# Kernel optimization log

Hardware: AMD Instinct MI355X
Metric: run time of the kernel (lower is better)

## Reference

```python
import jax, jax.numpy as jnp
import numpy as np

DIM, DEPTH, DH, CH, SH = 512, 2, 64, 2, 8
B, T, N = 8, 1024, 2048
CI, SI, FF = CH * DH, SH * DH, 4 * DIM


def layer_norm(x, w, b, eps=1e-5):
    m = jnp.mean(x, -1, keepdims=True)
    v = jnp.var(x, -1, keepdims=True)
    return (x - m) * jax.lax.rsqrt(v + eps) * w + b


def rotate_half(x):
    # interleaved pairs: (x0,x1) -> (-x1,x0)
    x1, x2 = x[..., 0::2], x[..., 1::2]
    return jnp.stack((-x2, x1), axis=-1).reshape(x.shape)


def apply_rot(freqs, x):
    return x * jnp.cos(freqs) + rotate_half(x) * jnp.sin(freqs)


def split_heads(x, h):
    b, t, _ = x.shape
    return x.reshape(b, t, h, -1).transpose(0, 2, 1, 3)


def merge_heads(x):
    b, h, t, d = x.shape
    return x.transpose(0, 2, 1, 3).reshape(b, t, h * d)


def rotary_attn(q, k, v, q_pos, k_pos, heads, mask=None):
    # q:(B,Tq,H*Dh), k/v:(B,Tk,H*Dh), pos:(B,T,Dh); rotate_value=False -> v untouched
    qh, kh, vh = split_heads(q, heads), split_heads(k, heads), split_heads(v, heads)
    qh = apply_rot(q_pos[:, None], qh)
    kh = apply_rot(k_pos[:, None], kh)
    scores = jnp.einsum('bhqd,bhkd->bhqk', qh, kh) * (DH ** -0.5)
    if mask is not None:
        scores = jnp.where(mask, scores, jnp.finfo(scores.dtype).min)
    attn = jax.nn.softmax(scores, axis=-1)
    return merge_heads(jnp.einsum('bhqk,bhkd->bhqd', attn, vh))


def _forward(bin_queries, bin_time_emb, encoder_latents, latent_time_emb,
             ca_lnq_w, ca_lnq_b, ca_lnc_w, ca_lnc_b, ca_wq, ca_wkv, ca_wo, ca_bo,
             sa_ln_w, sa_ln_b, sa_wqkv, sa_wo, sa_bo,
             ffn_ln_w, ffn_ln_b, ffn_w1, ffn_b1, ffn_w2, ffn_b2):
    Tq = bin_queries.shape[1]
    mask = jnp.tril(jnp.ones((Tq, Tq), dtype=bool))[None, None]  # (1,1,T,T) causal
    x = bin_queries
    for l in range(DEPTH):
        # 1) rotary cross-attention to history latents
        xn = layer_norm(x, ca_lnq_w[l], ca_lnq_b[l])
        cn = layer_norm(encoder_latents, ca_lnc_w[l], ca_lnc_b[l])
        q = xn @ ca_wq[l]
        k, v = jnp.split(cn @ ca_wkv[l], 2, axis=-1)
        x = x + rotary_attn(q, k, v, bin_time_emb, latent_time_emb, CH) @ ca_wo[l] + ca_bo[l]
        # 2) causal rotary self-attention over bin queries
        xn = layer_norm(x, sa_ln_w[l], sa_ln_b[l])
        q, k, v = jnp.split(xn @ sa_wqkv[l], 3, axis=-1)
        x = x + rotary_attn(q, k, v, bin_time_emb, bin_time_emb, SH, mask) @ sa_wo[l] + sa_bo[l]
        # 3) pre-LN FFN with GEGLU (mult=4), dropout off in eval
        h = layer_norm(x, ffn_ln_w[l], ffn_ln_b[l])
        a, g = jnp.split(h @ ffn_w1[l] + ffn_b1[l], 2, axis=-1)
        x = x + (a * jax.nn.gelu(g, approximate=False)) @ ffn_w2[l] + ffn_b2[l]
    return x


def setup_inputs() -> dict:
    key = jax.random.key(0)
    ks = jax.random.split(key, 12)
    n = lambda i, shape, s: jax.random.normal(ks[i], shape, dtype=jnp.float32) * s
    return {
        'bin_queries': n(0, (B, T, DIM), 1.0),
        'bin_time_emb': n(1, (B, T, DH), 1.0),
        'encoder_latents': n(2, (B, N, DIM), 1.0),
        'latent_time_emb': n(3, (B, N, DH), 1.0),
        'ca_lnq_w': jnp.ones((DEPTH, DIM)), 'ca_lnq_b': jnp.zeros((DEPTH, DIM)),
        'ca_lnc_w': jnp.ones((DEPTH, DIM)), 'ca_lnc_b': jnp.zeros((DEPTH, DIM)),
        'ca_wq': n(4, (DEPTH, DIM, CI), 0.02), 'ca_wkv': n(5, (DEPTH, DIM, 2 * CI), 0.02),
        'ca_wo': n(6, (DEPTH, CI, DIM), 0.02), 'ca_bo': jnp.zeros((DEPTH, DIM)),
        'sa_ln_w': jnp.ones((DEPTH, DIM)), 'sa_ln_b': jnp.zeros((DEPTH, DIM)),
        'sa_wqkv': n(7, (DEPTH, DIM, 3 * SI), 0.02), 'sa_wo': n(8, (DEPTH, SI, DIM), 0.02),
        'sa_bo': jnp.zeros((DEPTH, DIM)),
        'ffn_ln_w': jnp.ones((DEPTH, DIM)), 'ffn_ln_b': jnp.zeros((DEPTH, DIM)),
        'ffn_w1': n(9, (DEPTH, DIM, 2 * FF), 0.02), 'ffn_b1': jnp.zeros((DEPTH, 2 * FF)),
        'ffn_w2': n(10, (DEPTH, FF, DIM), 0.02), 'ffn_b2': jnp.zeros((DEPTH, DIM)),
    }


def reference(bin_queries, bin_time_emb, encoder_latents, latent_time_emb,
              ca_lnq_w, ca_lnq_b, ca_lnc_w, ca_lnc_b, ca_wq, ca_wkv, ca_wo, ca_bo,
              sa_ln_w, sa_ln_b, sa_wqkv, sa_wo, sa_bo,
              ffn_ln_w, ffn_ln_b, ffn_w1, ffn_b1, ffn_w2, ffn_b2):
    return _forward(bin_queries, bin_time_emb, encoder_latents, latent_time_emb,
                    ca_lnq_w, ca_lnq_b, ca_lnc_w, ca_lnc_b, ca_wq, ca_wkv, ca_wo, ca_bo,
                    sa_ln_w, sa_ln_b, sa_wqkv, sa_wo, sa_bo,
                    ffn_ln_w, ffn_ln_b, ffn_w1, ffn_b1, ffn_w2, ffn_b2)
```

## Files before the change

kernel.cpp:

```cpp
#include <hip/hip_runtime.h>
#include <cstdint>
#include <cstddef>

static constexpr int DIMc = 512;
static constexpr int DHc  = 64;
static constexpr int CHc  = 2;
static constexpr int SHc  = 8;
static constexpr int Bc   = 8;
static constexpr int Tc   = 1024;
static constexpr int Nc   = 2048;
static constexpr int CIc  = CHc * DHc;
static constexpr int SIc  = SHc * DHc;
static constexpr int FFc  = 4 * DIMc;
static constexpr int RQ   = Bc * Tc;
static constexpr int RL   = Bc * Nc;

typedef short bf16x8 __attribute__((ext_vector_type(8)));
typedef float f32x4  __attribute__((ext_vector_type(4)));

__device__ __forceinline__ ushort f2bf(float f) {
  uint32_t u = __builtin_bit_cast(uint32_t, f);
  u += 0x7fffu + ((u >> 16) & 1u);
  return (ushort)(u >> 16);
}
__device__ __forceinline__ uint32_t packbf2(float a, float b) {
  return (uint32_t)f2bf(a) | ((uint32_t)f2bf(b) << 16);
}
__device__ __forceinline__ float bf2f(ushort h) {
  uint32_t u = ((uint32_t)h) << 16;
  return __builtin_bit_cast(float, u);
}

__device__ __forceinline__ void gload_lds16(const ushort* g, ushort* lds) {
  __builtin_amdgcn_global_load_lds(
      (const __attribute__((address_space(1))) void*)g,
      (__attribute__((address_space(3))) void*)lds, 16, 0, 0);
}

__device__ __forceinline__ float gelu_fast(float g) {
  float u = g * (0.7978845608f + 0.0356774081f * g * g);
  float e = __expf(2.f * u);
  float th = 1.f - 2.f * __builtin_amdgcn_rcpf(1.f + e);
  return 0.5f * g * (1.f + th);
}

__global__ __launch_bounds__(256) void ln_rows(const float* __restrict__ X,
    const float* __restrict__ w, const float* __restrict__ b,
    ushort* __restrict__ out, int rows) {
  int gw = (int)((blockIdx.x * 256 + threadIdx.x) >> 6);
  int lane = threadIdx.x & 63;
  if (gw >= rows) return;
  const float* xr = X + (size_t)gw * DIMc;
  float4 v0 = *(const float4*)(xr + lane * 8);
  float4 v1 = *(const float4*)(xr + lane * 8 + 4);
  float xv[8] = {v0.x, v0.y, v0.z, v0.w, v1.x, v1.y, v1.z, v1.w};
  float s = 0.f, ss = 0.f;
#pragma unroll
  for (int i = 0; i < 8; i++) { s += xv[i]; ss += xv[i] * xv[i]; }
#pragma unroll
  for (int off = 32; off; off >>= 1) { s += __shfl_xor(s, off); ss += __shfl_xor(ss, off); }
  float mean = s * (1.f / DIMc);
  float var = ss * (1.f / DIMc) - mean * mean;
  float r = rsqrtf(var + 1e-5f);
  int c = lane * 8;
  ushort o[8] __attribute__((aligned(16)));
#pragma unroll
  for (int i = 0; i < 8; i++) o[i] = f2bf((xv[i] - mean) * r * w[c + i] + b[c + i]);
  *(uint4*)(out + (size_t)gw * DIMc + c) = *(const uint4*)o;
}

__global__ __launch_bounds__(256) void wtrans_all(
    const float* __restrict__ wq, const float* __restrict__ wkv,
    const float* __restrict__ wo, const float* __restrict__ qkv,
    const float* __restrict__ swo, const float* __restrict__ w1,
    const float* __restrict__ w2, ushort* __restrict__ dst, int layer) {
  constexpr int Ks[7]   = {512, 512, 128, 512, 512, 512, 2048};
  constexpr int Ns[7]   = {128, 256, 512, 1536, 512, 4096, 512};
  constexpr int pre[8]  = {0, 64, 192, 256, 1024, 1280, 3328, 4352};
  constexpr int dOff[7] = {0, 65536, 196608, 262144, 1048576, 1310720, 3407872};
  int bid = blockIdx.x;
  int wid = 0;
#pragma unroll
  for (int i = 1; i < 7; i++) wid += (bid >= pre[i]);
  int tileIdx = bid - pre[wid];
  int K = Ks[wid], N = Ns[wid];
  const float* srcs[7] = {wq, wkv, wo, qkv, swo, w1, w2};
  const float* W = srcs[wid] + (size_t)layer * K * N;
  ushort* Wt = dst + dOff[wid];
  int ntx = N / 32;
  int n0 = (tileIdx % ntx) * 32, k0 = (tileIdx / ntx) * 32;
  __shared__ float tile[32][33];
  int tx = threadIdx.x & 31, ty = threadIdx.x >> 5;
#pragma unroll
  for (int i = 0; i < 32; i += 8)
    tile[ty + i][tx] = W[(size_t)(k0 + ty + i) * N + n0 + tx];
  __syncthreads();
  if (wid == 5) {
#pragma unroll
    for (int i = 0; i < 32; i += 8) {
      int nrow = n0 + ty + i;
      int p = nrow & 2047;
      int rowT = ((p >> 4) << 5) + ((nrow < 2048) ? 0 : 16) + (p & 15);
      Wt[(size_t)rowT * K + k0 + tx] = f2bf(tile[tx][ty + i]);
    }
  } else {
#pragma unroll
    for (int i = 0; i < 32; i += 8)
      Wt[(size_t)(n0 + ty + i) * K + k0 + tx] = f2bf(tile[tx][ty + i]);
  }
}

__global__ __launch_bounds__(256) void vtrans(const ushort* __restrict__ src,
    ushort* __restrict__ dst, int NK, int stride, int colOff) {
  __shared__ ushort tile[32][33];
  int b = blockIdx.z;
  int key0 = blockIdx.x * 32, hd0 = blockIdx.y * 32;
  int HD = gridDim.y * 32;
  int tx = threadIdx.x & 31, ty = threadIdx.x >> 5;
#pragma unroll
  for (int i = 0; i < 32; i += 8)
    tile[ty + i][tx] = src[(size_t)(b * NK + key0 + ty + i) * stride + colOff + hd0 + tx];
  __syncthreads();
#pragma unroll
  for (int i = 0; i < 32; i += 8)
    dst[((size_t)b * HD + hd0 + ty + i) * NK + key0 + tx] = tile[tx][ty + i];
}

template<int MODE>
__global__ __launch_bounds__(256) void gemm128(const ushort* __restrict__ A,
    const ushort* __restrict__ Bt, const float* __restrict__ bias,
    const float* __restrict__ resIn, float* __restrict__ resOut,
    ushort* __restrict__ outB, int M, int N, int K) {
  __shared__ __align__(16) ushort As[128 * 64];
  __shared__ __align__(16) ushort Bs[128 * 64];
  int t = threadIdx.x, wv = t >> 6, lane = t & 63;
  int bm = blockIdx.y, bn = blockIdx.x;
  int fr = lane & 15, g = lane >> 4;
  int wr = (wv >> 1) * 64, wc = (wv & 1) * 64;
  int srow = wv * 32 + (lane >> 3);
  int sslot = lane & 7;
  const ushort* Abase = A + (size_t)(bm * 128) * K;
  const ushort* Bbase = Bt + (size_t)(bn * 128) * K;

  f32x4 acc[4][4] = {};
  for (int k0 = 0; k0 < K; k0 += 64) {
#pragma unroll
    for (int j = 0; j < 4; j++) {
      int r = srow + j * 8;
      int kc = sslot ^ (r & 7);
      gload_lds16(Abase + (size_t)r * K + k0 + kc * 8, As + (wv * 256 + j * 64) * 8);
      gload_lds16(Bbase + (size_t)r * K + k0 + kc * 8, Bs + (wv * 256 + j * 64) * 8);
    }
    __syncthreads();
#pragma unroll
    for (int ks = 0; ks < 2; ks++) {
      bf16x8 af[4], bf[4];
#pragma unroll
      for (int mm = 0; mm < 4; mm++) {
        int row = wr + mm * 16 + fr;
        af[mm] = *(const bf16x8*)(As + row * 64 + (((ks * 4 + g) ^ (row & 7)) * 8));
      }
#pragma unroll
      for (int nn = 0; nn < 4; nn++) {
        int row = wc + nn * 16 + fr;
        bf[nn] = *(const bf16x8*)(Bs + row * 64 + (((ks * 4 + g) ^ (row & 7)) * 8));
      }
#pragma unroll
      for (int mm = 0; mm < 4; mm++)
#pragma unroll
        for (int nn = 0; nn < 4; nn++)
          acc[mm][nn] = __builtin_amdgcn_mfma_f32_16x16x32_bf16(af[mm], bf[nn], acc[mm][nn], 0, 0, 0);
    }
    __syncthreads();
  }

  if (MODE == 2) {
    int NH = N >> 1;
#pragma unroll
    for (int mm = 0; mm < 4; mm++)
#pragma unroll
      for (int np = 0; np < 2; np++) {
        int ocol = bn * 64 + (wc >> 1) + np * 16 + fr;
        float ba = bias[ocol];
        float bg = bias[NH + ocol];
#pragma unroll
        for (int i = 0; i < 4; i++) {
          int gr = bm * 128 + wr + mm * 16 + g * 4 + i;
          float a = acc[mm][np * 2][i] + ba;
          float gv = acc[mm][np * 2 + 1][i] + bg;
          outB[(size_t)gr * NH + ocol] = f2bf(a * gelu_fast(gv));
        }
      }
  } else {
#pragma unroll
    for (int mm = 0; mm < 4; mm++)
#pragma unroll
      for (int nn = 0; nn < 4; nn++)
#pragma unroll
        for (int i = 0; i < 4; i++) {
          int gr = bm * 128 + wr + mm * 16 + g * 4 + i;
          int gc = bn * 128 + wc + nn * 16 + fr;
          float val = acc[mm][nn][i] + (bias ? bias[gc] : 0.f);
          if (MODE == 0) outB[(size_t)gr * N + gc] = f2bf(val);
          else resOut[(size_t)gr * N + gc] = resIn[(size_t)gr * N + gc] + val;
        }
  }
}

template<int MODE>
__global__ __launch_bounds__(256) void gemm128x64(const ushort* __restrict__ A,
    const ushort* __restrict__ Bt, const float* __restrict__ bias,
    const float* __restrict__ resIn, float* __restrict__ resOut,
    ushort* __restrict__ outB, int M, int N, int K) {
  __shared__ __align__(16) ushort As[128 * 64];
  __shared__ __align__(16) ushort Bs[64 * 64];
  int t = threadIdx.x, wv = t >> 6, lane = t & 63;
  int bm = blockIdx.y, bn = blockIdx.x;
  int fr = lane & 15, g = lane >> 4;
  int wr = (wv >> 1) * 64, wc = (wv & 1) * 32;
  const ushort* Abase = A + (size_t)(bm * 128) * K;
  const ushort* Bbase = Bt + (size_t)(bn * 64) * K;

  f32x4 acc[4][2] = {};
  for (int k0 = 0; k0 < K; k0 += 64) {
#pragma unroll
    for (int j = 0; j < 4; j++) {
      int c = j * 256 + wv * 64 + lane;
      int r = c >> 3, s = c & 7;
      int kc = s ^ (r & 7);
      gload_lds16(Abase + (size_t)r * K + k0 + kc * 8, As + (j * 256 + wv * 64) * 8);
      if (j < 2)
        gload_lds16(Bbase + (size_t)r * K + k0 + kc * 8, Bs + (j * 256 + wv * 64) * 8);
    }
    __syncthreads();
#pragma unroll
    for (int ks = 0; ks < 2; ks++) {
      bf16x8 af[4], bf[2];
#pragma unroll
      for (int mm = 0; mm < 4; mm++) {
        int row = wr + mm * 16 + fr;
        af[mm] = *(const bf16x8*)(As + row * 64 + (((ks * 4 + g) ^ (row & 7)) * 8));
      }
#pragma unroll
      for (int nn = 0; nn < 2; nn++) {
        int row = wc + nn * 16 + fr;
        bf[nn] = *(const bf16x8*)(Bs + row * 64 + (((ks * 4 + g) ^ (row & 7)) * 8));
      }
#pragma unroll
      for (int mm = 0; mm < 4; mm++)
#pragma unroll
        for (int nn = 0; nn < 2; nn++)
          acc[mm][nn] = __builtin_amdgcn_mfma_f32_16x16x32_bf16(af[mm], bf[nn], acc[mm][nn], 0, 0, 0);
    }
    __syncthreads();
  }

#pragma unroll
  for (int mm = 0; mm < 4; mm++)
#pragma unroll
    for (int nn = 0; nn < 2; nn++)
#pragma unroll
      for (int i = 0; i < 4; i++) {
        int gr = bm * 128 + wr + mm * 16 + g * 4 + i;
        int gc = bn * 64 + wc + nn * 16 + fr;
        float val = acc[mm][nn][i] + (bias ? bias[gc] : 0.f);
        if (MODE == 0) outB[(size_t)gr * N + gc] = f2bf(val);
        else resOut[(size_t)gr * N + gc] = resIn[(size_t)gr * N + gc] + val;
      }
}

template<int MODE>
__global__ __launch_bounds__(256) void gemm64(const ushort* __restrict__ A,
    const ushort* __restrict__ Bt, const float* __restrict__ bias,
    float* __restrict__ resF, ushort* __restrict__ outB,
    int M, int N, int K) {
  __shared__ __align__(16) ushort As[64][40];
  __shared__ __align__(16) ushort Bs[64][40];
  int t = threadIdx.x;
  int bm = blockIdx.y, bn = blockIdx.x;
  int row = t >> 2, kc = (t & 3) << 3;
  const ushort* aG = A + (size_t)(bm * 64 + row) * K + kc;
  const ushort* bG = Bt + (size_t)(bn * 64 + row) * K + kc;
  int wv = t >> 6, lane = t & 63;
  int wr = (wv >> 1) * 32, wc = (wv & 1) * 32;
  int fr = lane & 15, fk = (lane >> 4) << 3;
  f32x4 acc[2][2] = {};
  for (int k0 = 0; k0 < K; k0 += 32) {
    *(uint4*)&As[row][kc] = *(const uint4*)(aG + k0);
    *(uint4*)&Bs[row][kc] = *(const uint4*)(bG + k0);
    __syncthreads();
    bf16x8 a0 = *(const bf16x8*)&As[wr + fr][fk];
    bf16x8 a1 = *(const bf16x8*)&As[wr + 16 + fr][fk];
    bf16x8 b0 = *(const bf16x8*)&Bs[wc + fr][fk];
    bf16x8 b1 = *(const bf16x8*)&Bs[wc + 16 + fr][fk];
    acc[0][0] = __builtin_amdgcn_mfma_f32_16x16x32_bf16(a0, b0, acc[0][0], 0, 0, 0);
    acc[0][1] = __builtin_amdgcn_mfma_f32_16x16x32_bf16(a0, b1, acc[0][1], 0, 0, 0);
    acc[1][0] = __builtin_amdgcn_mfma_f32_16x16x32_bf16(a1, b0, acc[1][0], 0, 0, 0);
    acc[1][1] = __builtin_amdgcn_mfma_f32_16x16x32_bf16(a1, b1, acc[1][1], 0, 0, 0);
    __syncthreads();
  }
  int cr0 = wr + ((lane >> 4) << 2);
  int cc0 = wc + fr;
#pragma unroll
  for (int mm = 0; mm < 2; mm++)
#pragma unroll
    for (int nn = 0; nn < 2; nn++)
#pragma unroll
      for (int i = 0; i < 4; i++) {
        int gr = bm * 64 + cr0 + mm * 16 + i;
        int gc = bn * 64 + cc0 + nn * 16;
        float val = acc[mm][nn][i] + (bias ? bias[gc] : 0.f);
        if (MODE == 0) outB[(size_t)gr * N + gc] = f2bf(val);
        else resF[(size_t)gr * N + gc] = resF[(size_t)gr * N + gc] + val;
      }
}

__global__ __launch_bounds__(256) void rope_apply(ushort* __restrict__ buf,
    const float* __restrict__ fr, int rows, int stride, int colOff, int H, float scale) {
  int idx = blockIdx.x * 256 + threadIdx.x;
  int total = rows * H * 32;
  if (idx >= total) return;
  int p = idx & 31;
  int h = (idx >> 5) % H;
  int r = idx / (32 * H);
  float f0 = fr[(size_t)r * DHc + 2 * p];
  float f1 = fr[(size_t)r * DHc + 2 * p + 1];
  ushort* bp = buf + (size_t)r * stride + colOff + h * DHc + 2 * p;
  float x0 = bf2f(bp[0]), x1 = bf2f(bp[1]);
  float o0 = (x0 * __cosf(f0) - x1 * __sinf(f0)) * scale;
  float o1 = (x1 * __cosf(f1) + x0 * __sinf(f1)) * scale;
  bp[0] = f2bf(o0); bp[1] = f2bf(o1);
}

template<int CAUSAL>
__global__ __launch_bounds__(256) void attn_mfma(
    const ushort* __restrict__ Q, const ushort* __restrict__ K,
    const ushort* __restrict__ Vt, ushort* __restrict__ O,
    int qStride, int kStride, int kOff, int oStride,
    int Tq, int NK, int H) {
  __shared__ __align__(16) ushort Ks[64 * 64];
  __shared__ __align__(16) ushort Vs[64 * 64];
  __shared__ __align__(16) ushort Ps[4][16 * 72];
  int b = blockIdx.z, h = blockIdx.y;
  int qt = CAUSAL ? ((int)gridDim.x - 1 - (int)blockIdx.x) : blockIdx.x;
  int t = threadIdx.x, wv = t >> 6, lane = t & 63;
  int g = lane >> 4, fr = lane & 15;
  int qw = qt * 64 + wv * 16;
  int HD = H * 64;

  const ushort* qrow = Q + (size_t)(b * Tq + qw + fr) * qStride + h * 64;
  bf16x8 qlo = *(const bf16x8*)(qrow + g * 8);
  bf16x8 qhi = *(const bf16x8*)(qrow + 32 + g * 8);

  f32x4 o_acc[4] = {};
  float m_run = -1e30f, l_run = 0.f;

  uint32_t* Pw = (uint32_t*)&Ps[wv][0];
  int ntiles = CAUSAL ? (qt + 1) : (NK / 64);
  for (int kt = 0; kt < ntiles; kt++) {
    int k0 = kt * 64;
    __syncthreads();
#pragma unroll
    for (int i = 0; i < 2; i++) {
      int id = t + i * 256;
      int r = id >> 3, c = id & 7;
      uint4 kval = *(const uint4*)(K + (size_t)(b * NK + k0 + r) * kStride + kOff + h * 64 + c * 8);
      *(uint4*)(Ks + r * 64 + ((c ^ (r & 7)) * 8)) = kval;
      uint4 vval = *(const uint4*)(Vt + ((size_t)b * HD + h * 64 + r) * NK + k0 + c * 8);
      *(uint4*)(Vs + r * 64 + ((c ^ (r & 7)) * 8)) = vval;
    }
    __syncthreads();

    f32x4 s[4];
#pragma unroll
    for (int nn = 0; nn < 4; nn++) {
      int row = nn * 16 + fr;
      bf16x8 kf0 = *(const bf16x8*)(Ks + row * 64 + ((g ^ (fr & 7)) * 8));
      bf16x8 kf1 = *(const bf16x8*)(Ks + row * 64 + (((4 + g) ^ (fr & 7)) * 8));
      f32x4 z = {};
      z = __builtin_amdgcn_mfma_f32_16x16x32_bf16(kf0, qlo, z, 0, 0, 0);
      z = __builtin_amdgcn_mfma_f32_16x16x32_bf16(kf1, qhi, z, 0, 0, 0);
      s[nn] = z;
    }
    if (CAUSAL && (k0 + 63 > qw)) {
#pragma unroll
      for (int nn = 0; nn < 4; nn++)
#pragma unroll
        for (int i = 0; i < 4; i++)
          if (k0 + nn * 16 + g * 4 + i > qw + fr) s[nn][i] = -1e30f;
    }
    float tm = s[0][0];
#pragma unroll
    for (int nn = 0; nn < 4; nn++)
#pragma unroll
      for (int i = 0; i < 4; i++) tm = fmaxf(tm, s[nn][i]);
    tm = fmaxf(tm, __shfl_xor(tm, 16));
    tm = fmaxf(tm, __shfl_xor(tm, 32));
    float mnew = fmaxf(m_run, tm);
    float corr = __expf(m_run - mnew);
    float ps = 0.f;
#pragma unroll
    for (int nn = 0; nn < 4; nn++)
#pragma unroll
      for (int i = 0; i < 4; i++) {
        float p = __expf(s[nn][i] - mnew);
        s[nn][i] = p;
        ps += p;
      }
    ps += __shfl_xor(ps, 16);
    ps += __shfl_xor(ps, 32);
    l_run = l_run * corr + ps;
    m_run = mnew;
#pragma unroll
    for (int dd = 0; dd < 4; dd++) o_acc[dd] *= corr;
#pragma unroll
    for (int nn = 0; nn < 4; nn++)
#pragma unroll
      for (int p = 0; p < 2; p++)
        Pw[fr * 36 + 8 * nn + 2 * g + p] = packbf2(s[nn][2 * p], s[nn][2 * p + 1]);
    bf16x8 pa0 = *(const bf16x8*)(&Ps[wv][fr * 72 + g * 8]);
    bf16x8 pa1 = *(const bf16x8*)(&Ps[wv][fr * 72 + 32 + g * 8]);
#pragma unroll
    for (int dd = 0; dd < 4; dd++) {
      int row = dd * 16 + fr;
      bf16x8 vf0 = *(const bf16x8*)(Vs + row * 64 + ((g ^ (fr & 7)) * 8));
      bf16x8 vf1 = *(const bf16x8*)(Vs + row * 64 + (((4 + g) ^ (fr & 7)) * 8));
      o_acc[dd] = __builtin_amdgcn_mfma_f32_16x16x32_bf16(vf0, pa0, o_acc[dd], 0, 0, 0);
      o_acc[dd] = __builtin_amdgcn_mfma_f32_16x16x32_bf16(vf1, pa1, o_acc[dd], 0, 0, 0);
    }
  }
  float rl = 1.f / l_run;
  ushort* obase = O + (size_t)(b * Tq + qw + fr) * oStride + h * 64;
#pragma unroll
  for (int dd = 0; dd < 4; dd++) {
    uint2 w;
    w.x = packbf2(o_acc[dd][0] * rl, o_acc[dd][1] * rl);
    w.y = packbf2(o_acc[dd][2] * rl, o_acc[dd][3] * rl);
    *(uint2*)(obase + dd * 16 + g * 4) = w;
  }
}

extern "C" void kernel_launch(void* const* d_in, const int* in_sizes, int n_in,
                              void* d_out, int out_size, void* d_ws, size_t ws_size,
                              hipStream_t stream) {
  const float* bin_queries = (const float*)d_in[0];
  const float* bin_time    = (const float*)d_in[1];
  const float* latents     = (const float*)d_in[2];
  const float* lat_time    = (const float*)d_in[3];
  const float* ca_lnq_w = (const float*)d_in[4];
  const float* ca_lnq_b = (const float*)d_in[5];
  const float* ca_lnc_w = (const float*)d_in[6];
  const float* ca_lnc_b = (const float*)d_in[7];
  const float* ca_wq  = (const float*)d_in[8];
  const float* ca_wkv = (const float*)d_in[9];
  const float* ca_wo  = (const float*)d_in[10];
  const float* ca_bo  = (const float*)d_in[11];
  const float* sa_ln_w = (const float*)d_in[12];
  const float* sa_ln_b = (const float*)d_in[13];
  const float* sa_wqkv = (const float*)d_in[14];
  const float* sa_wo   = (const float*)d_in[15];
  const float* sa_bo   = (const float*)d_in[16];
  const float* ffn_ln_w = (const float*)d_in[17];
  const float* ffn_ln_b = (const float*)d_in[18];
  const float* ffn_w1 = (const float*)d_in[19];
  const float* ffn_b1 = (const float*)d_in[20];
  const float* ffn_w2 = (const float*)d_in[21];
  const float* ffn_b2 = (const float*)d_in[22];

  constexpr size_t X_BYTES = (size_t)RQ * DIMc * 4;
  char* ws = (char*)d_ws;
  float* x = (float*)ws;
  char* A0 = ws + X_BYTES;
  ushort* cn     = (ushort*)(A0);
  ushort* ca_xn  = (ushort*)(A0 + 16777216);
  ushort* qbuf   = (ushort*)(A0 + 25165824);
  ushort* kv     = (ushort*)(A0 + 27262976);
  ushort* ca_att = (ushort*)(A0 + 35651584);
  ushort* vt_c   = (ushort*)(A0 + 37748736);
  ushort* sa_xn  = (ushort*)(A0);
  ushort* qkv    = (ushort*)(A0 + 8388608);
  ushort* sa_att = (ushort*)(A0 + 33554432);
  ushort* vt_s   = (ushort*)(A0 + 41943040);
  ushort* hb     = (ushort*)(A0);
  ushort* ag     = (ushort*)(A0 + 8388608);
  char* W0 = A0 + 109051904;
  ushort* wbase = (ushort*)W0;
  ushort* wqT  = wbase;
  ushort* wkvT = wbase + 65536;
  ushort* woT  = wbase + 196608;
  ushort* qkvT = wbase + 262144;
  ushort* swoT = wbase + 1048576;
  ushort* w1T  = wbase + 1310720;
  ushort* w2T  = wbase + 3407872;

  hipMemcpyAsync(x, bin_queries, X_BYTES, hipMemcpyDeviceToDevice, stream);

  for (int l = 0; l < 2; l++) {
    wtrans_all<<<4352, 256, 0, stream>>>(ca_wq, ca_wkv, ca_wo, sa_wqkv, sa_wo,
                                         ffn_w1, ffn_w2, wbase, l);

    ln_rows<<<RQ / 4, 256, 0, stream>>>(x, ca_lnq_w + l * DIMc, ca_lnq_b + l * DIMc, ca_xn, RQ);
    ln_rows<<<RL / 4, 256, 0, stream>>>(latents, ca_lnc_w + l * DIMc, ca_lnc_b + l * DIMc, cn, RL);
    gemm64<0><<<dim3(CIc / 64, RQ / 64), 256, 0, stream>>>(ca_xn, wqT, nullptr, nullptr, qbuf, RQ, CIc, DIMc);
    gemm128x64<0><<<dim3(2 * CIc / 64, RL / 128), 256, 0, stream>>>(cn, wkvT, nullptr,
        nullptr, nullptr, kv, RL, 2 * CIc, DIMc);
    rope_apply<<<(RQ * CHc * 32) / 256, 256, 0, stream>>>(qbuf, bin_time, RQ, CIc, 0, CHc, 0.125f);
    rope_apply<<<(RL * CHc * 32) / 256, 256, 0, stream>>>(kv, lat_time, RL, 2 * CIc, 0, CHc, 1.f);
    vtrans<<<dim3(Nc / 32, CHc * 64 / 32, Bc), 256, 0, stream>>>(kv, vt_c, Nc, 2 * CIc, CIc);
    attn_mfma<0><<<dim3(Tc / 64, CHc, Bc), 256, 0, stream>>>(qbuf, kv, vt_c, ca_att,
        CIc, 2 * CIc, 0, CIc, Tc, Nc, CHc);
    gemm128x64<1><<<dim3(DIMc / 64, RQ / 128), 256, 0, stream>>>(ca_att, woT, ca_bo + l * DIMc,
        x, x, nullptr, RQ, DIMc, CIc);

    ln_rows<<<RQ / 4, 256, 0, stream>>>(x, sa_ln_w + l * DIMc, sa_ln_b + l * DIMc, sa_xn, RQ);
    gemm128<0><<<dim3(3 * SIc / 128, RQ / 128), 256, 0, stream>>>(sa_xn, qkvT, nullptr,
        nullptr, nullptr, qkv, RQ, 3 * SIc, DIMc);
    rope_apply<<<(RQ * SHc * 32) / 256, 256, 0, stream>>>(qkv, bin_time, RQ, 3 * SIc, 0, SHc, 0.125f);
    rope_apply<<<(RQ * SHc * 32) / 256, 256, 0, stream>>>(qkv, bin_time, RQ, 3 * SIc, SIc, SHc, 1.f);
    vtrans<<<dim3(Tc / 32, SHc * 64 / 32, Bc), 256, 0, stream>>>(qkv, vt_s, Tc, 3 * SIc, 2 * SIc);
    attn_mfma<1><<<dim3(Tc / 64, SHc, Bc), 256, 0, stream>>>(qkv, qkv, vt_s, sa_att,
        3 * SIc, 3 * SIc, SIc, SIc, Tc, Tc, SHc);
    gemm128x64<1><<<dim3(DIMc / 64, RQ / 128), 256, 0, stream>>>(sa_att, swoT, sa_bo + l * DIMc,
        x, x, nullptr, RQ, DIMc, SIc);

    ln_rows<<<RQ / 4, 256, 0, stream>>>(x, ffn_ln_w + l * DIMc, ffn_ln_b + l * DIMc, hb, RQ);
    gemm128<2><<<dim3(2 * FFc / 128, RQ / 128), 256, 0, stream>>>(hb, w1T,
        ffn_b1 + (size_t)l * 2 * FFc, nullptr, nullptr, ag, RQ, 2 * FFc, DIMc);
    float* resOut = (l == 1) ? (float*)d_out : x;
    gemm128x64<1><<<dim3(DIMc / 64, RQ / 128), 256, 0, stream>>>(ag, w2T, ffn_b2 + l * DIMc,
        x, resOut, nullptr, RQ, DIMc, FFc);
  }
}
```

Measured before the change: 685.7 us.

## Fuse rotary embedding and V transpose into projection GEMM epilogues

```diff
diff --git a/kernel.cpp b/kernel.cpp
--- a/kernel.cpp
+++ b/kernel.cpp
@@ -44,6 +44,19 @@
   return 0.5f * g * (1.f + th);
 }
 
+__device__ __forceinline__ float rope_rot(int odd, float v, float p, float2 cs) {
+  return odd ? (v * cs.x + p * cs.y) : (v * cs.x - p * cs.y);
+}
+
+__global__ __launch_bounds__(256) void trig_prep(const float* __restrict__ src,
+    float2* __restrict__ dst, int n) {
+  int i = blockIdx.x * 256 + threadIdx.x;
+  if (i >= n) return;
+  float s, c;
+  __sincosf(src[i], &s, &c);
+  dst[i] = make_float2(c, s);
+}
+
 __global__ __launch_bounds__(256) void ln_rows(const float* __restrict__ X,
     const float* __restrict__ w, const float* __restrict__ b,
     ushort* __restrict__ out, int rows) {
@@ -110,27 +123,12 @@
   }
 }
 
-__global__ __launch_bounds__(256) void vtrans(const ushort* __restrict__ src,
-    ushort* __restrict__ dst, int NK, int stride, int colOff) {
-  __shared__ ushort tile[32][33];
-  int b = blockIdx.z;
-  int key0 = blockIdx.x * 32, hd0 = blockIdx.y * 32;
-  int HD = gridDim.y * 32;
-  int tx = threadIdx.x & 31, ty = threadIdx.x >> 5;
-#pragma unroll
-  for (int i = 0; i < 32; i += 8)
-    tile[ty + i][tx] = src[(size_t)(b * NK + key0 + ty + i) * stride + colOff + hd0 + tx];
-  __syncthreads();
-#pragma unroll
-  for (int i = 0; i < 32; i += 8)
-    dst[((size_t)b * HD + hd0 + ty + i) * NK + key0 + tx] = tile[tx][ty + i];
-}
-
 template<int MODE>
 __global__ __launch_bounds__(256) void gemm128(const ushort* __restrict__ A,
     const ushort* __restrict__ Bt, const float* __restrict__ bias,
     const float* __restrict__ resIn, float* __restrict__ resOut,
-    ushort* __restrict__ outB, int M, int N, int K) {
+    ushort* __restrict__ outB, int M, int N, int K,
+    const float2* __restrict__ cs, ushort* __restrict__ vt) {
   __shared__ __align__(16) ushort As[128 * 64];
   __shared__ __align__(16) ushort Bs[128 * 64];
   int t = threadIdx.x, wv = t >> 6, lane = t & 63;
@@ -191,6 +189,39 @@
           outB[(size_t)gr * NH + ocol] = f2bf(a * gelu_fast(gv));
         }
       }
+  } else if (MODE == 3) {
+    if (bn * 128 < 1024) {
+#pragma unroll
+      for (int mm = 0; mm < 4; mm++)
+#pragma unroll
+        for (int nn = 0; nn < 4; nn++) {
+          int gc = bn * 128 + wc + nn * 16 + fr;
+          int d = gc & 63;
+          float sc = (gc < 512) ? 0.125f : 1.f;
+#pragma unroll
+          for (int i = 0; i < 4; i++) {
+            int gr = bm * 128 + wr + mm * 16 + g * 4 + i;
+            float val = acc[mm][nn][i];
+            float prt = __shfl_xor(val, 1);
+            float2 csv = cs[(size_t)gr * 64 + d];
+            outB[(size_t)gr * N + gc] = f2bf(rope_rot(fr & 1, val, prt, csv) * sc);
+          }
+        }
+    } else {
+#pragma unroll
+      for (int mm = 0; mm < 4; mm++)
+#pragma unroll
+        for (int nn = 0; nn < 4; nn++) {
+          int gc = bn * 128 + wc + nn * 16 + fr;
+          int ch = gc - 1024;
+          int gr0 = bm * 128 + wr + mm * 16 + g * 4;
+          int bb = gr0 >> 10, t0 = gr0 & 1023;
+          uint2 w;
+          w.x = packbf2(acc[mm][nn][0], acc[mm][nn][1]);
+          w.y = packbf2(acc[mm][nn][2], acc[mm][nn][3]);
+          *(uint2*)(vt + ((size_t)bb * 512 + ch) * 1024 + t0) = w;
+        }
+    }
   } else {
 #pragma unroll
     for (int mm = 0; mm < 4; mm++)
@@ -211,7 +242,8 @@
 __global__ __launch_bounds__(256) void gemm128x64(const ushort* __restrict__ A,
     const ushort* __restrict__ Bt, const float* __restrict__ bias,
     const float* __restrict__ resIn, float* __restrict__ resOut,
-    ushort* __restrict__ outB, int M, int N, int K) {
+    ushort* __restrict__ outB, int M, int N, int K,
+    const float2* __restrict__ cs, ushort* __restrict__ vt) {
   __shared__ __align__(16) ushort As[128 * 64];
   __shared__ __align__(16) ushort Bs[64 * 64];
   int t = threadIdx.x, wv = t >> 6, lane = t & 63;
@@ -255,25 +287,57 @@
     __syncthreads();
   }
 
-#pragma unroll
-  for (int mm = 0; mm < 4; mm++)
-#pragma unroll
-    for (int nn = 0; nn < 2; nn++)
-#pragma unroll
-      for (int i = 0; i < 4; i++) {
-        int gr = bm * 128 + wr + mm * 16 + g * 4 + i;
-        int gc = bn * 64 + wc + nn * 16 + fr;
-        float val = acc[mm][nn][i] + (bias ? bias[gc] : 0.f);
-        if (MODE == 0) outB[(size_t)gr * N + gc] = f2bf(val);
-        else resOut[(size_t)gr * N + gc] = resIn[(size_t)gr * N + gc] + val;
-      }
-}
-
-template<int MODE>
-__global__ __launch_bounds__(256) void gemm64(const ushort* __restrict__ A,
-    const ushort* __restrict__ Bt, const float* __restrict__ bias,
-    float* __restrict__ resF, ushort* __restrict__ outB,
-    int M, int N, int K) {
+  if (MODE == 3) {
+    if (bn * 64 < 128) {
+#pragma unroll
+      for (int mm = 0; mm < 4; mm++)
+#pragma unroll
+        for (int nn = 0; nn < 2; nn++) {
+          int gc = bn * 64 + wc + nn * 16 + fr;
+          int d = gc & 63;
+#pragma unroll
+          for (int i = 0; i < 4; i++) {
+            int gr = bm * 128 + wr + mm * 16 + g * 4 + i;
+            float val = acc[mm][nn][i];
+            float prt = __shfl_xor(val, 1);
+            float2 csv = cs[(size_t)gr * 64 + d];
+            outB[(size_t)gr * N + gc] = f2bf(rope_rot(fr & 1, val, prt, csv));
+          }
+        }
+    } else {
+#pragma unroll
+      for (int mm = 0; mm < 4; mm++)
+#pragma unroll
+        for (int nn = 0; nn < 2; nn++) {
+          int gc = bn * 64 + wc + nn * 16 + fr;
+          int ch = gc - 128;
+          int gr0 = bm * 128 + wr + mm * 16 + g * 4;
+          int bb = gr0 >> 11, t0 = gr0 & 2047;
+          uint2 w;
+          w.x = packbf2(acc[mm][nn][0], acc[mm][nn][1]);
+          w.y = packbf2(acc[mm][nn][2], acc[mm][nn][3]);
+          *(uint2*)(vt + ((size_t)bb * 128 + ch) * 2048 + t0) = w;
+        }
+    }
+  } else {
+#pragma unroll
+    for (int mm = 0; mm < 4; mm++)
+#pragma unroll
+      for (int nn = 0; nn < 2; nn++)
+#pragma unroll
+        for (int i = 0; i < 4; i++) {
+          int gr = bm * 128 + wr + mm * 16 + g * 4 + i;
+          int gc = bn * 64 + wc + nn * 16 + fr;
+          float val = acc[mm][nn][i] + (bias ? bias[gc] : 0.f);
+          if (MODE == 0) outB[(size_t)gr * N + gc] = f2bf(val);
+          else resOut[(size_t)gr * N + gc] = resIn[(size_t)gr * N + gc] + val;
+        }
+  }
+}
+
+__global__ __launch_bounds__(256) void gemm64_rope(const ushort* __restrict__ A,
+    const ushort* __restrict__ Bt, ushort* __restrict__ outB,
+    const float2* __restrict__ cs, int M, int N, int K) {
   __shared__ __align__(16) ushort As[64][40];
   __shared__ __align__(16) ushort Bs[64][40];
   int t = threadIdx.x;
@@ -304,32 +368,18 @@
 #pragma unroll
   for (int mm = 0; mm < 2; mm++)
 #pragma unroll
-    for (int nn = 0; nn < 2; nn++)
+    for (int nn = 0; nn < 2; nn++) {
+      int gc = bn * 64 + cc0 + nn * 16;
+      int d = gc & 63;
 #pragma unroll
       for (int i = 0; i < 4; i++) {
         int gr = bm * 64 + cr0 + mm * 16 + i;
-        int gc = bn * 64 + cc0 + nn * 16;
-        float val = acc[mm][nn][i] + (bias ? bias[gc] : 0.f);
-        if (MODE == 0) outB[(size_t)gr * N + gc] = f2bf(val);
-        else resF[(size_t)gr * N + gc] = resF[(size_t)gr * N + gc] + val;
-      }
-}
-
-__global__ __launch_bounds__(256) void rope_apply(ushort* __restrict__ buf,
-    const float* __restrict__ fr, int rows, int stride, int colOff, int H, float scale) {
-  int idx = blockIdx.x * 256 + threadIdx.x;
-  int total = rows * H * 32;
-  if (idx >= total) return;
-  int p = idx & 31;
-  int h = (idx >> 5) % H;
-  int r = idx / (32 * H);
-  float f0 = fr[(size_t)r * DHc + 2 * p];
-  float f1 = fr[(size_t)r * DHc + 2 * p + 1];
-  ushort* bp = buf + (size_t)r * stride + colOff + h * DHc + 2 * p;
-  float x0 = bf2f(bp[0]), x1 = bf2f(bp[1]);
-  float o0 = (x0 * __cosf(f0) - x1 * __sinf(f0)) * scale;
-  float o1 = (x1 * __cosf(f1) + x0 * __sinf(f1)) * scale;
-  bp[0] = f2bf(o0); bp[1] = f2bf(o1);
+        float val = acc[mm][nn][i];
+        float prt = __shfl_xor(val, 1);
+        float2 csv = cs[(size_t)gr * 64 + d];
+        outB[(size_t)gr * N + gc] = f2bf(rope_rot(fr & 1, val, prt, csv) * 0.125f);
+      }
+    }
 }
 
 template<int CAUSAL>
@@ -483,6 +533,8 @@
   ushort* vt_s   = (ushort*)(A0 + 41943040);
   ushort* hb     = (ushort*)(A0);
   ushort* ag     = (ushort*)(A0 + 8388608);
+  float2* csQ = (float2*)(A0 + 62914560);
+  float2* csL = (float2*)(A0 + 67108864);
   char* W0 = A0 + 109051904;
   ushort* wbase = (ushort*)W0;
   ushort* wqT  = wbase;
@@ -493,41 +545,37 @@
   ushort* w1T  = wbase + 1310720;
   ushort* w2T  = wbase + 3407872;
 
-  hipMemcpyAsync(x, bin_queries, X_BYTES, hipMemcpyDeviceToDevice, stream);
+  trig_prep<<<(RQ * 64) / 256, 256, 0, stream>>>(bin_time, csQ, RQ * 64);
+  trig_prep<<<(RL * 64) / 256, 256, 0, stream>>>(lat_time, csL, RL * 64);
 
   for (int l = 0; l < 2; l++) {
     wtrans_all<<<4352, 256, 0, stream>>>(ca_wq, ca_wkv, ca_wo, sa_wqkv, sa_wo,
                                          ffn_w1, ffn_w2, wbase, l);
 
-    ln_rows<<<RQ / 4, 256, 0, stream>>>(x, ca_lnq_w + l * DIMc, ca_lnq_b + l * DIMc, ca_xn, RQ);
+    const float* xin = (l == 0) ? bin_queries : x;
+    ln_rows<<<RQ / 4, 256, 0, stream>>>(xin, ca_lnq_w + l * DIMc, ca_lnq_b + l * DIMc, ca_xn, RQ);
     ln_rows<<<RL / 4, 256, 0, stream>>>(latents, ca_lnc_w + l * DIMc, ca_lnc_b + l * DIMc, cn, RL);
-    gemm64<0><<<dim3(CIc / 64, RQ / 64), 256, 0, stream>>>(ca_xn, wqT, nullptr, nullptr, qbuf, RQ, CIc, DIMc);
-    gemm128x64<0><<<dim3(2 * CIc / 64, RL / 128), 256, 0, stream>>>(cn, wkvT, nullptr,
-        nullptr, nullptr, kv, RL, 2 * CIc, DIMc);
-    rope_apply<<<(RQ * CHc * 32) / 256, 256, 0, stream>>>(qbuf, bin_time, RQ, CIc, 0, CHc, 0.125f);
-    rope_apply<<<(RL * CHc * 32) / 256, 256, 0, stream>>>(kv, lat_time, RL, 2 * CIc, 0, CHc, 1.f);
-    vtrans<<<dim3(Nc / 32, CHc * 64 / 32, Bc), 256, 0, stream>>>(kv, vt_c, Nc, 2 * CIc, CIc);
+    gemm64_rope<<<dim3(CIc / 64, RQ / 64), 256, 0, stream>>>(ca_xn, wqT, qbuf, csQ, RQ, CIc, DIMc);
+    gemm128x64<3><<<dim3(2 * CIc / 64, RL / 128), 256, 0, stream>>>(cn, wkvT, nullptr,
+        nullptr, nullptr, kv, RL, 2 * CIc, DIMc, csL, vt_c);
     attn_mfma<0><<<dim3(Tc / 64, CHc, Bc), 256, 0, stream>>>(qbuf, kv, vt_c, ca_att,
         CIc, 2 * CIc, 0, CIc, Tc, Nc, CHc);
     gemm128x64<1><<<dim3(DIMc / 64, RQ / 128), 256, 0, stream>>>(ca_att, woT, ca_bo + l * DIMc,
-        x, x, nullptr, RQ, DIMc, CIc);
+        xin, x, nullptr, RQ, DIMc, CIc, nullptr, nullptr);
 
     ln_rows<<<RQ / 4, 256, 0, stream>>>(x, sa_ln_w + l * DIMc, sa_ln_b + l * DIMc, sa_xn, RQ);
-    gemm128<0><<<dim3(3 * SIc / 128, RQ / 128), 256, 0, stream>>>(sa_xn, qkvT, nullptr,
-        nullptr, nullptr, qkv, RQ, 3 * SIc, DIMc);
-    rope_apply<<<(RQ * SHc * 32) / 256, 256, 0, stream>>>(qkv, bin_time, RQ, 3 * SIc, 0, SHc, 0.125f);
-    rope_apply<<<(RQ * SHc * 32) / 256, 256, 0, stream>>>(qkv, bin_time, RQ, 3 * SIc, SIc, SHc, 1.f);
-    vtrans<<<dim3(Tc / 32, SHc * 64 / 32, Bc), 256, 0, stream>>>(qkv, vt_s, Tc, 3 * SIc, 2 * SIc);
+    gemm128<3><<<dim3(3 * SIc / 128, RQ / 128), 256, 0, stream>>>(sa_xn, qkvT, nullptr,
+        nullptr, nullptr, qkv, RQ, 3 * SIc, DIMc, csQ, vt_s);
     attn_mfma<1><<<dim3(Tc / 64, SHc, Bc), 256, 0, stream>>>(qkv, qkv, vt_s, sa_att,
         3 * SIc, 3 * SIc, SIc, SIc, Tc, Tc, SHc);
     gemm128x64<1><<<dim3(DIMc / 64, RQ / 128), 256, 0, stream>>>(sa_att, swoT, sa_bo + l * DIMc,
-        x, x, nullptr, RQ, DIMc, SIc);
+        x, x, nullptr, RQ, DIMc, SIc, nullptr, nullptr);
 
     ln_rows<<<RQ / 4, 256, 0, stream>>>(x, ffn_ln_w + l * DIMc, ffn_ln_b + l * DIMc, hb, RQ);
     gemm128<2><<<dim3(2 * FFc / 128, RQ / 128), 256, 0, stream>>>(hb, w1T,
-        ffn_b1 + (size_t)l * 2 * FFc, nullptr, nullptr, ag, RQ, 2 * FFc, DIMc);
+        ffn_b1 + (size_t)l * 2 * FFc, nullptr, nullptr, ag, RQ, 2 * FFc, DIMc, nullptr, nullptr);
     float* resOut = (l == 1) ? (float*)d_out : x;
     gemm128x64<1><<<dim3(DIMc / 64, RQ / 128), 256, 0, stream>>>(ag, w2T, ffn_b2 + l * DIMc,
-        x, resOut, nullptr, RQ, DIMc, FFc);
-  }
-}
+        x, resOut, nullptr, RQ, DIMc, FFc, nullptr, nullptr);
+  }
+}
```

After: 634.1 us. -7.5%, faster.
